# Kernel optimization log

Hardware: AMD Instinct MI355X
Metric: run time of the kernel (lower is better)

Reference implementation:

```python
import jax, jax.numpy as jnp
import numpy as np

N_NODES = 100000


def gcn_conv(h, W, b, src, dst, n):
    # h: [N, Fin] -> [N, Fout], GCNConv with symmetric normalization + self-loops
    h = h @ W  # transform first (PyG order): [N, Fout]
    loop = jnp.arange(n, dtype=src.dtype)
    src_sl = jnp.concatenate([src, loop])  # [E+N]
    dst_sl = jnp.concatenate([dst, loop])
    deg = jax.ops.segment_sum(jnp.ones_like(dst_sl, dtype=h.dtype), dst_sl, num_segments=n)  # [N]
    dinv = jax.lax.rsqrt(deg)  # deg >= 1 thanks to self-loops
    norm = dinv[src_sl] * dinv[dst_sl]  # [E+N]
    msgs = h[src_sl] * norm[:, None]  # gather + scale: [E+N, Fout]
    out = jax.ops.segment_sum(msgs, dst_sl, num_segments=n)  # scatter-add
    return out + b


def setup_inputs() -> dict:
    key = jax.random.key(0)
    kx, ke, k1, k2 = jax.random.split(key, 4)
    in_dim, hid_dim, out_dim = 512, 128, 40
    x = jax.random.normal(kx, (N_NODES, in_dim), dtype=jnp.float32)
    edge_index = jax.random.randint(ke, (2, 1600000), 0, N_NODES, dtype=jnp.int64)
    s1 = 1.0 / np.sqrt(in_dim)
    s2 = 1.0 / np.sqrt(hid_dim)
    W1 = jax.random.uniform(k1, (in_dim, hid_dim), jnp.float32, -s1, s1)
    b1 = jnp.zeros((hid_dim,), jnp.float32)
    W2 = jax.random.uniform(k2, (hid_dim, out_dim), jnp.float32, -s2, s2)
    b2 = jnp.zeros((out_dim,), jnp.float32)
    return {"x": x, "edge_index": edge_index, "W1": W1, "b1": b1, "W2": W2, "b2": b2}


def reference(x, edge_index, W1, b1, W2, b2):
    src, dst = edge_index[0], edge_index[1]
    n = x.shape[0]
    h = jax.nn.relu(gcn_conv(x, W1, b1, src, dst, n))
    h = gcn_conv(h, W2, b2, src, dst, n)
    return jax.nn.log_softmax(h, axis=1)
```

## Files before the change

kernel.cpp:

```cpp
#include <hip/hip_runtime.h>
#include <math.h>

#define FIN 512
#define FH 128
#define FOUT 40
#define FP 64
#define NB 512
#define PSLOTS 30
#define CAPG 4096
#define PBLK 512

typedef unsigned char u8;
typedef __attribute__((ext_vector_type(8))) short bf16x8;
typedef __attribute__((ext_vector_type(4))) float f32x4;
typedef __attribute__((ext_vector_type(2))) float f32x2;

__device__ inline ushort f2bf(float f){
  union { float f; uint32_t u; } v; v.f = f;
  uint32_t u = v.u;
  uint32_t r = (u + 0x7FFF + ((u >> 16) & 1)) >> 16;
  return (ushort)r;
}
__device__ inline uint32_t cvtpk(float a, float b){
  uint32_t r;
  asm("v_cvt_pk_bf16_f32 %0, %1, %2" : "=v"(r) : "v"(a), "v"(b));
  return r;
}
__device__ inline f32x2 pkadd(f32x2 a, f32x2 b){
  f32x2 r;
  asm("v_pk_add_f32 %0, %1, %2" : "=v"(r) : "v"(a), "v"(b));
  return r;
}
__device__ inline f32x2 f8lo(uint32_t v){ return __builtin_amdgcn_cvt_pk_f32_fp8(v, false); }
__device__ inline f32x2 f8hi(uint32_t v){ return __builtin_amdgcn_cvt_pk_f32_fp8(v, true); }
__device__ inline u8 f2f8(float v){
  return (u8)(__builtin_amdgcn_cvt_pk_fp8_f32(v, v, 0, false) & 0xFF);
}

__global__ __launch_bounds__(256) void k_part(const int* __restrict__ src,
                                              const int* __restrict__ dst, int e,
                                              int* __restrict__ gcur,
                                              uint32_t* __restrict__ gbuf, int n, int npb,
                                              const float* __restrict__ W1,
                                              const float* __restrict__ W2,
                                              ushort* __restrict__ W1t, ushort* __restrict__ W2t){
  __shared__ uint32_t pbuf[NB*PSLOTS];
  __shared__ int lcnt[NB];
  int b = blockIdx.x, t = threadIdx.x;
  int gidx = b*256 + t;
  if(gidx < FIN*FH){
    int k = gidx / FH, c = gidx % FH;
    W1t[(size_t)c*FIN + k] = f2bf(W1[gidx]);
  }
  if(gidx < 48*FH){
    int c = gidx / FH, k = gidx % FH;
    W2t[gidx] = (c < FOUT) ? f2bf(W2[(size_t)k*FOUT + c]) : (ushort)0;
  }
  for(int i=t;i<NB;i+=256) lcnt[i]=0;
  __syncthreads();
  int chunk = (e + PBLK - 1) / PBLK;
  int base = b * chunk;
  int endE = base + chunk; if(endE > e) endE = e;
  if(base >= e) return;
  int rounds = (endE - base + 255) / 256;
  for(int rr=0; rr<rounds; ++rr){
    int i = base + rr*256 + t;
    if(i < endE){
      int s = src[i];
      int d = dst[i];
      int bk = d / npb;
      uint32_t pk_ = ((uint32_t)s << 8) | (uint32_t)(d - bk*npb);
      int slot = atomicAdd(&lcnt[bk], 1);
      if(slot < PSLOTS){
        pbuf[bk*PSLOTS + slot] = pk_;
      } else {
        int g = atomicAdd(&gcur[bk], 1);
        gbuf[(size_t)bk*CAPG + g] = pk_;
      }
    }
    __syncthreads();
    bool last = (rr == rounds-1);
    for(int tb=t; tb<NB; tb+=256){
      int c = lcnt[tb];
      int k = c < PSLOTS ? c : PSLOTS;
      if(k > 0 && (k >= 16 || last)){
        int g = atomicAdd(&gcur[tb], k);
        uint32_t* dstp = &gbuf[(size_t)tb*CAPG + g];
        const uint32_t* srcp = &pbuf[tb*PSLOTS];
        for(int q=0; q<k; q++) dstp[q] = srcp[q];
        lcnt[tb] = 0;
      }
    }
    __syncthreads();
  }
}

__global__ __launch_bounds__(256) void k_hist(const uint32_t* __restrict__ gbuf,
                                              const int* __restrict__ gcur,
                                              int* __restrict__ rp, float* __restrict__ dinv,
                                              int* __restrict__ aux, int n, int npb){
  __shared__ int hist[256];
  __shared__ int sh[256];
  int b = blockIdx.x, t = threadIdx.x;
  int base = b * npb;
  if(base >= n){ if(t==0) aux[b] = 0; return; }
  hist[t] = 0;
  __syncthreads();
  int m = gcur[b];
  const uint32_t* bp = gbuf + (size_t)b*CAPG;
  for(int i=t; i<m; i+=256) atomicAdd(&hist[bp[i] & 255u], 1);
  __syncthreads();
  int v = hist[t];
  sh[t] = v;
  __syncthreads();
  for(int off=1; off<256; off<<=1){
    int x = (t>=off)? sh[t-off]:0; __syncthreads();
    sh[t]+=x; __syncthreads();
  }
  int nn = n - base; if(nn > npb) nn = npb;
  if(t < nn){
    rp[base+t+1] = sh[t];
    dinv[base+t] = rsqrtf((float)(v+1));
  }
  if(t==255) aux[b] = sh[255];
}

__global__ __launch_bounds__(512) void k_scan_c(int* __restrict__ rp, const int* __restrict__ aux,
                                                int n, int npb){
  __shared__ int sh[512];
  int t = threadIdx.x;
  sh[t] = aux[t];
  __syncthreads();
  for(int off=1; off<512; off<<=1){
    int x = (t>=off)? sh[t-off]:0; __syncthreads();
    sh[t]+=x; __syncthreads();
  }
  int i = blockIdx.x*512 + t;
  if(i<n){
    int b = i / npb;
    int add = (b>0)? sh[b-1] : 0;
    rp[i+1] += add;
  }
  if(i==0) rp[0] = 0;
}

__global__ __launch_bounds__(512, 2) void k_gemm1(const float* __restrict__ X,
                                                  const ushort* __restrict__ W1t,
                                                  const float* __restrict__ dinv,
                                                  u8* __restrict__ XWs, int n){
  __shared__ char smem[65536];
  int t = threadIdx.x;
  int gi = blockIdx.x;
  int lane = t & 63;
  int wid = t >> 6;
  int l15 = lane & 15;
  int lk8 = (lane >> 4) * 8;
  int rowbase = gi * 256 + wid * 32;

  int r0 = rowbase + l15;      if (r0 >= n) r0 = n-1;
  int r1 = rowbase + 16 + l15; if (r1 >= n) r1 = n-1;
  const float* a0p = X + (size_t)r0*FIN;
  const float* a1p = X + (size_t)r1*FIN;

  f32x4 acc[2][8];
  #pragma unroll
  for(int i=0;i<2;i++)
    #pragma unroll
    for(int j=0;j<8;j++) acc[i][j] = (f32x4){0.f,0.f,0.f,0.f};

  char* WsB = smem;

  #pragma unroll
  for(int half=0; half<2; half++){
    if(half) __syncthreads();
    #pragma unroll
    for(int it=0; it<8; it++){
      int c = it*512 + t;
      int col = c >> 5, kslot = c & 31;
      uint4 v = *(const uint4*)(W1t + (size_t)col*FIN + half*256 + kslot*8);
      int dstb = col*512 + ((kslot*16) ^ ((col & 7) << 4));
      *(uint4*)(WsB + dstb) = v;
    }
    __syncthreads();

    for(int kc=0; kc<8; kc++){
      int kl = kc*32 + lk8;
      int kg = half*256 + kl;
      float4 a0a = *(const float4*)(a0p + kg);
      float4 a0b = *(const float4*)(a0p + kg + 4);
      float4 a1a = *(const float4*)(a1p + kg);
      float4 a1b = *(const float4*)(a1p + kg + 4);
      uint4 fa0u, fa1u;
      fa0u.x = cvtpk(a0a.x, a0a.y); fa0u.y = cvtpk(a0a.z, a0a.w);
      fa0u.z = cvtpk(a0b.x, a0b.y); fa0u.w = cvtpk(a0b.z, a0b.w);
      fa1u.x = cvtpk(a1a.x, a1a.y); fa1u.y = cvtpk(a1a.z, a1a.w);
      fa1u.z = cvtpk(a1b.x, a1b.y); fa1u.w = cvtpk(a1b.z, a1b.w);
      bf16x8 fa0 = *(bf16x8*)&fa0u;
      bf16x8 fa1 = *(bf16x8*)&fa1u;

      #pragma unroll
      for(int fj=0; fj<8; fj++){
        int col = fj*16 + l15;
        int srcb = col*512 + ((kl*2) ^ ((col & 7) << 4));
        bf16x8 fb = *(const bf16x8*)(WsB + srcb);
        acc[0][fj] = __builtin_amdgcn_mfma_f32_16x16x32_bf16(fa0, fb, acc[0][fj], 0, 0, 0);
        acc[1][fj] = __builtin_amdgcn_mfma_f32_16x16x32_bf16(fa1, fb, acc[1][fj], 0, 0, 0);
      }
    }
  }

  int rbase = (lane >> 4) * 4;
  #pragma unroll
  for(int fi=0; fi<2; fi++){
    #pragma unroll
    for(int r=0; r<4; r++){
      int row = rowbase + fi*16 + rbase + r;
      if(row < n){
        float dd = dinv[row];
        #pragma unroll
        for(int fj=0; fj<8; fj++){
          XWs[(size_t)row*FH + fj*16 + l15] = f2f8(acc[fi][fj][r] * dd);
        }
      }
    }
  }
}

__global__ __launch_bounds__(512) void k_fill2(const uint32_t* __restrict__ gbuf,
                                               const int* __restrict__ gcur,
                                               const int* __restrict__ rp,
                                               int* __restrict__ srcs, int n, int npb){
  __shared__ int lcur[256];
  int fb = blockIdx.x;
  int t = threadIdx.x;
  int base = fb * npb;
  if(base >= n) return;
  int nn = n - base; if(nn > npb) nn = npb;
  for(int i = t; i < nn; i += 512) lcur[i] = rp[base + i];
  __syncthreads();
  int m = gcur[fb];
  const uint32_t* bp = gbuf + (size_t)fb*CAPG;
  for(int i = t; i < m; i += 512){
    uint32_t v = bp[i];
    int ld = (int)(v & 255u);
    int p = atomicAdd(&lcur[ld], 1);
    srcs[p] = (int)(v >> 8);
  }
}

__global__ __launch_bounds__(256) void k_agg1(const u8* __restrict__ XWs, const int* __restrict__ rp,
                                              const int* __restrict__ srcs, const float* __restrict__ dinv,
                                              const float* __restrict__ b1, ushort* __restrict__ H1b, int n){
  int d = blockIdx.x*4 + (threadIdx.x >> 6);
  if(d >= n) return;
  int lane = threadIdx.x & 63;
  int g = lane >> 3, li = lane & 7;
  f32x2 acc[8];
  #pragma unroll
  for(int k=0;k<8;k++) acc[k] = (f32x2){0.f,0.f};
  int beg = rp[d];
  int end = rp[d+1];
  int j = beg + g;
  bool h0 = j < end, h1 = j + 8 < end;
  int s0 = 0, s1 = 0;
  if(h0) s0 = srcs[j];
  if(h1) s1 = srcs[j+8];
  while(h1){
    int nj = j + 16;
    bool nh0 = nj < end, nh1 = nj + 8 < end;
    int ns0 = 0, ns1 = 0;
    if(nh0) ns0 = srcs[nj];
    if(nh1) ns1 = srcs[nj+8];
    uint4 a0 = *(const uint4*)(XWs + (size_t)s0*FH + li*16);
    uint4 c0 = *(const uint4*)(XWs + (size_t)s1*FH + li*16);
    acc[0] = pkadd(acc[0], pkadd(f8lo(a0.x), f8lo(c0.x)));
    acc[1] = pkadd(acc[1], pkadd(f8hi(a0.x), f8hi(c0.x)));
    acc[2] = pkadd(acc[2], pkadd(f8lo(a0.y), f8lo(c0.y)));
    acc[3] = pkadd(acc[3], pkadd(f8hi(a0.y), f8hi(c0.y)));
    acc[4] = pkadd(acc[4], pkadd(f8lo(a0.z), f8lo(c0.z)));
    acc[5] = pkadd(acc[5], pkadd(f8hi(a0.z), f8hi(c0.z)));
    acc[6] = pkadd(acc[6], pkadd(f8lo(a0.w), f8lo(c0.w)));
    acc[7] = pkadd(acc[7], pkadd(f8hi(a0.w), f8hi(c0.w)));
    j = nj; s0 = ns0; s1 = ns1; h0 = nh0; h1 = nh1;
  }
  if(h0){
    uint4 a0 = *(const uint4*)(XWs + (size_t)s0*FH + li*16);
    acc[0] = pkadd(acc[0], f8lo(a0.x));
    acc[1] = pkadd(acc[1], f8hi(a0.x));
    acc[2] = pkadd(acc[2], f8lo(a0.y));
    acc[3] = pkadd(acc[3], f8hi(a0.y));
    acc[4] = pkadd(acc[4], f8lo(a0.z));
    acc[5] = pkadd(acc[5], f8hi(a0.z));
    acc[6] = pkadd(acc[6], f8lo(a0.w));
    acc[7] = pkadd(acc[7], f8hi(a0.w));
  }
  #pragma unroll
  for(int k=0;k<8;k++){
    #pragma unroll
    for(int c=0;c<2;c++){
      acc[k][c] += __shfl_xor(acc[k][c], 8);
      acc[k][c] += __shfl_xor(acc[k][c], 16);
      acc[k][c] += __shfl_xor(acc[k][c], 32);
    }
  }
  if(g == 0){
    uint4 sv4 = *(const uint4*)(XWs + (size_t)d*FH + li*16);
    f32x2 slf[8];
    slf[0]=f8lo(sv4.x); slf[1]=f8hi(sv4.x); slf[2]=f8lo(sv4.y); slf[3]=f8hi(sv4.y);
    slf[4]=f8lo(sv4.z); slf[5]=f8hi(sv4.z); slf[6]=f8lo(sv4.w); slf[7]=f8hi(sv4.w);
    float dd = dinv[d];
    uint32_t w[8];
    #pragma unroll
    for(int k=0;k<8;k++){
      float b0 = b1[li*16 + k*2];
      float b1v = b1[li*16 + k*2 + 1];
      float o0 = fmaxf((acc[k][0]+slf[k][0])*dd + b0, 0.f);
      float o1 = fmaxf((acc[k][1]+slf[k][1])*dd + b1v, 0.f);
      w[k] = cvtpk(o0, o1);
    }
    uint4 w0 = {w[0],w[1],w[2],w[3]};
    uint4 w1 = {w[4],w[5],w[6],w[7]};
    uint4* wp = (uint4*)(H1b + (size_t)d*FH + li*16);
    wp[0] = w0;
    wp[1] = w1;
  }
}

__global__ __launch_bounds__(256) void k_gemm2_mfma(const ushort* __restrict__ H1b,
                                                    const ushort* __restrict__ W2t,
                                                    const float* __restrict__ dinv,
                                                    u8* __restrict__ H2s, int n){
  int t = threadIdx.x;
  int lane = t & 63;
  int wid = t >> 6;
  int l15 = lane & 15;
  int lk8 = (lane >> 4) * 8;
  int rowbase = blockIdx.x * 128 + wid * 32;

  int r0 = rowbase + l15;      if (r0 >= n) r0 = n-1;
  int r1 = rowbase + 16 + l15; if (r1 >= n) r1 = n-1;
  const ushort* a0p = H1b + (size_t)r0*FH + lk8;
  const ushort* a1p = H1b + (size_t)r1*FH + lk8;

  f32x4 acc[2][3];
  #pragma unroll
  for(int i=0;i<2;i++)
    #pragma unroll
    for(int j=0;j<3;j++) acc[i][j] = (f32x4){0.f,0.f,0.f,0.f};

  #pragma unroll
  for(int kc=0; kc<4; kc++){
    int k0 = kc*32;
    bf16x8 fa0 = *(const bf16x8*)(a0p + k0);
    bf16x8 fa1 = *(const bf16x8*)(a1p + k0);
    #pragma unroll
    for(int fj=0; fj<3; fj++){
      bf16x8 fb = *(const bf16x8*)(W2t + (size_t)(fj*16 + l15)*FH + k0 + lk8);
      acc[0][fj] = __builtin_amdgcn_mfma_f32_16x16x32_bf16(fa0, fb, acc[0][fj], 0, 0, 0);
      acc[1][fj] = __builtin_amdgcn_mfma_f32_16x16x32_bf16(fa1, fb, acc[1][fj], 0, 0, 0);
    }
  }

  int rbase = (lane >> 4) * 4;
  #pragma unroll
  for(int fi=0; fi<2; fi++){
    #pragma unroll
    for(int r=0; r<4; r++){
      int row = rowbase + fi*16 + rbase + r;
      if(row < n){
        float dd = dinv[row];
        #pragma unroll
        for(int fj=0; fj<3; fj++){
          int col = fj*16 + l15;
          H2s[(size_t)row*FP + col] = (col < FOUT) ? f2f8(acc[fi][fj][r] * dd) : (u8)0;
        }
        H2s[(size_t)row*FP + 48 + l15] = (u8)0;
      }
    }
  }
}

__global__ __launch_bounds__(256) void k_agg2_sm(const u8* __restrict__ H2s, const int* __restrict__ rp,
                                                 const int* __restrict__ srcs, const float* __restrict__ dinv,
                                                 const float* __restrict__ b2, float* __restrict__ out, int n){
  int d = blockIdx.x*4 + (threadIdx.x >> 6);
  if(d >= n) return;
  int lane = threadIdx.x & 63;
  int g = lane >> 3, li = lane & 7;
  f32x2 acc[4];
  #pragma unroll
  for(int k=0;k<4;k++) acc[k] = (f32x2){0.f,0.f};
  int beg = rp[d];
  int end = rp[d+1];
  int j = beg + g;
  bool h0 = j < end, h1 = j + 8 < end;
  int s0 = 0, s1 = 0;
  if(h0) s0 = srcs[j];
  if(h1) s1 = srcs[j+8];
  while(h1){
    int nj = j + 16;
    bool nh0 = nj < end, nh1 = nj + 8 < end;
    int ns0 = 0, ns1 = 0;
    if(nh0) ns0 = srcs[nj];
    if(nh1) ns1 = srcs[nj+8];
    uint2 v = *(const uint2*)(H2s + (size_t)s0*FP + li*8);
    uint2 u = *(const uint2*)(H2s + (size_t)s1*FP + li*8);
    acc[0] = pkadd(acc[0], pkadd(f8lo(v.x), f8lo(u.x)));
    acc[1] = pkadd(acc[1], pkadd(f8hi(v.x), f8hi(u.x)));
    acc[2] = pkadd(acc[2], pkadd(f8lo(v.y), f8lo(u.y)));
    acc[3] = pkadd(acc[3], pkadd(f8hi(v.y), f8hi(u.y)));
    j = nj; s0 = ns0; s1 = ns1; h0 = nh0; h1 = nh1;
  }
  if(h0){
    uint2 v = *(const uint2*)(H2s + (size_t)s0*FP + li*8);
    acc[0] = pkadd(acc[0], f8lo(v.x));
    acc[1] = pkadd(acc[1], f8hi(v.x));
    acc[2] = pkadd(acc[2], f8lo(v.y));
    acc[3] = pkadd(acc[3], f8hi(v.y));
  }
  #pragma unroll
  for(int k=0;k<4;k++){
    #pragma unroll
    for(int c=0;c<2;c++){
      acc[k][c] += __shfl_xor(acc[k][c], 8);
      acc[k][c] += __shfl_xor(acc[k][c], 16);
      acc[k][c] += __shfl_xor(acc[k][c], 32);
    }
  }
  uint2 sv = *(const uint2*)(H2s + (size_t)d*FP + li*8);
  f32x2 s2[4] = { f8lo(sv.x), f8hi(sv.x), f8lo(sv.y), f8hi(sv.y) };
  float dd = dinv[d];
  float val[8];
  #pragma unroll
  for(int k=0;k<4;k++){
    #pragma unroll
    for(int c=0;c<2;c++){
      int col = li*8 + k*2 + c;
      float bv = (col < FOUT) ? b2[col] : 0.f;
      val[k*2+c] = (col < FOUT) ? ((acc[k][c]+s2[k][c])*dd + bv) : -3.402823466e38f;
    }
  }
  float m = val[0];
  #pragma unroll
  for(int k=1;k<8;k++) m = fmaxf(m, val[k]);
  #pragma unroll
  for(int off=1; off<8; off<<=1) m = fmaxf(m, __shfl_xor(m, off));
  float ssum = 0.f;
  #pragma unroll
  for(int k=0;k<8;k++){
    int col = li*8 + k;
    ssum += (col < FOUT) ? expf(val[k] - m) : 0.f;
  }
  #pragma unroll
  for(int off=1; off<8; off<<=1) ssum += __shfl_xor(ssum, off);
  float lse = m + logf(ssum);
  if(g == 0 && li < 5){
    float4 o0 = {val[0]-lse, val[1]-lse, val[2]-lse, val[3]-lse};
    float4 o1 = {val[4]-lse, val[5]-lse, val[6]-lse, val[7]-lse};
    float* op = out + (size_t)d*FOUT + li*8;
    *(float4*)op = o0;
    *(float4*)(op+4) = o1;
  }
}


extern "C" void kernel_launch(void* const* d_in, const int* in_sizes, int n_in,
                              void* d_out, int out_size, void* d_ws, size_t ws_size,
                              hipStream_t stream){
  const float* X  = (const float*)d_in[0];
  const int*   ei = (const int*)d_in[1];
  const float* W1 = (const float*)d_in[2];
  const float* b1 = (const float*)d_in[3];
  const float* W2 = (const float*)d_in[4];
  const float* b2 = (const float*)d_in[5];
  float* out = (float*)d_out;

  int n = in_sizes[0] / FIN;
  int e = in_sizes[1] / 2;
  const int* src = ei;
  const int* dst = ei + e;

  int npb = (n + NB - 1) / NB;

  u8* XWs     = (u8*)d_ws;
  ushort* H1b = (ushort*)(XWs + (size_t)n*FH);
  u8* H2s     = (u8*)(H1b + (size_t)n*FH);
  ushort* W1t = (ushort*)(H2s + (size_t)n*FP);
  ushort* W2t = W1t + (size_t)FH*FIN;
  float* dinv = (float*)(W2t + 48*FH);
  int* gcur   = (int*)(dinv + n);
  int* rp     = gcur + NB;
  int* srcs   = rp + (n+1) + 3;
  int* aux    = srcs + e;
  uint32_t* gbuf = (uint32_t*)H1b;

  int G = (n + 255) / 256;

  hipMemsetAsync(gcur, 0, (size_t)NB*sizeof(int), stream);
  hipLaunchKernelGGL(k_part, dim3(PBLK), dim3(256), 0, stream,
                     src, dst, e, gcur, gbuf, n, npb, W1, W2, W1t, W2t);
  hipLaunchKernelGGL(k_hist, dim3(NB), dim3(256), 0, stream, gbuf, gcur, rp, dinv, aux, n, npb);
  hipLaunchKernelGGL(k_scan_c, dim3((n+511)/512), dim3(512), 0, stream, rp, aux, n, npb);

  hipLaunchKernelGGL(k_gemm1, dim3(G), dim3(512), 0, stream, X, W1t, dinv, XWs, n);
  hipLaunchKernelGGL(k_fill2, dim3(NB), dim3(512), 0, stream, gbuf, gcur, rp, srcs, n, npb);

  hipLaunchKernelGGL(k_agg1, dim3((n+3)/4), dim3(256), 0, stream, XWs, rp, srcs, dinv, b1, H1b, n);
  hipLaunchKernelGGL(k_gemm2_mfma, dim3((n+127)/128), dim3(256), 0, stream, H1b, W2t, dinv, H2s, n);
  hipLaunchKernelGGL(k_agg2_sm, dim3((n+3)/4), dim3(256), 0, stream, H2s, rp, srcs, dinv, b2, out, n);
}
```

Baseline: 247.9 us.

## Simplify edge partition to direct global atomics and fuse histogram with CSR fill

The partition kernel drops its shared-memory staging buffers. Each edge now goes straight into its dst bucket in the global buffer through a global atomic, using one thread per edge. The block-offset scan now runs on the bucket counts in a single small kernel, and the per-bucket histogram is fused with the CSR source fill, removing the separate scan and fill launches. This cuts launches and a pass over the bucket buffer, but adds heavy global atomic contention on 512 counters across 1.6M edges.

```diff
diff --git a/kernel.cpp b/kernel.cpp
--- a/kernel.cpp
+++ b/kernel.cpp
@@ -6,9 +6,7 @@
 #define FOUT 40
 #define FP 64
 #define NB 512
-#define PSLOTS 30
 #define CAPG 4096
-#define PBLK 512
 
 typedef unsigned char u8;
 typedef __attribute__((ext_vector_type(8))) short bf16x8;
@@ -44,66 +42,50 @@
                                               const float* __restrict__ W1,
                                               const float* __restrict__ W2,
                                               ushort* __restrict__ W1t, ushort* __restrict__ W2t){
-  __shared__ uint32_t pbuf[NB*PSLOTS];
-  __shared__ int lcnt[NB];
-  int b = blockIdx.x, t = threadIdx.x;
-  int gidx = b*256 + t;
-  if(gidx < FIN*FH){
-    int k = gidx / FH, c = gidx % FH;
-    W1t[(size_t)c*FIN + k] = f2bf(W1[gidx]);
-  }
-  if(gidx < 48*FH){
-    int c = gidx / FH, k = gidx % FH;
-    W2t[gidx] = (c < FOUT) ? f2bf(W2[(size_t)k*FOUT + c]) : (ushort)0;
-  }
-  for(int i=t;i<NB;i+=256) lcnt[i]=0;
+  int i = blockIdx.x*256 + threadIdx.x;
+  if(i < FIN*FH){
+    int k = i / FH, c = i % FH;
+    W1t[(size_t)c*FIN + k] = f2bf(W1[i]);
+  }
+  if(i < 48*FH){
+    int c = i / FH, k = i % FH;
+    W2t[i] = (c < FOUT) ? f2bf(W2[(size_t)k*FOUT + c]) : (ushort)0;
+  }
+  if(i < e){
+    int s = src[i];
+    int d = dst[i];
+    int bk = d / npb;
+    uint32_t pk_ = ((uint32_t)s << 8) | (uint32_t)(d - bk*npb);
+    int p = atomicAdd(&gcur[bk], 1);
+    gbuf[(size_t)bk*CAPG + p] = pk_;
+  }
+}
+
+__global__ __launch_bounds__(512) void k_scan_g(const int* __restrict__ gcur,
+                                                int* __restrict__ bstart){
+  __shared__ int sh[512];
+  int t = threadIdx.x;
+  sh[t] = gcur[t];
   __syncthreads();
-  int chunk = (e + PBLK - 1) / PBLK;
-  int base = b * chunk;
-  int endE = base + chunk; if(endE > e) endE = e;
-  if(base >= e) return;
-  int rounds = (endE - base + 255) / 256;
-  for(int rr=0; rr<rounds; ++rr){
-    int i = base + rr*256 + t;
-    if(i < endE){
-      int s = src[i];
-      int d = dst[i];
-      int bk = d / npb;
-      uint32_t pk_ = ((uint32_t)s << 8) | (uint32_t)(d - bk*npb);
-      int slot = atomicAdd(&lcnt[bk], 1);
-      if(slot < PSLOTS){
-        pbuf[bk*PSLOTS + slot] = pk_;
-      } else {
-        int g = atomicAdd(&gcur[bk], 1);
-        gbuf[(size_t)bk*CAPG + g] = pk_;
-      }
-    }
-    __syncthreads();
-    bool last = (rr == rounds-1);
-    for(int tb=t; tb<NB; tb+=256){
-      int c = lcnt[tb];
-      int k = c < PSLOTS ? c : PSLOTS;
-      if(k > 0 && (k >= 16 || last)){
-        int g = atomicAdd(&gcur[tb], k);
-        uint32_t* dstp = &gbuf[(size_t)tb*CAPG + g];
-        const uint32_t* srcp = &pbuf[tb*PSLOTS];
-        for(int q=0; q<k; q++) dstp[q] = srcp[q];
-        lcnt[tb] = 0;
-      }
-    }
-    __syncthreads();
-  }
-}
-
-__global__ __launch_bounds__(256) void k_hist(const uint32_t* __restrict__ gbuf,
-                                              const int* __restrict__ gcur,
-                                              int* __restrict__ rp, float* __restrict__ dinv,
-                                              int* __restrict__ aux, int n, int npb){
+  for(int off=1; off<512; off<<=1){
+    int x = (t>=off)? sh[t-off]:0; __syncthreads();
+    sh[t]+=x; __syncthreads();
+  }
+  bstart[t] = (t>0)? sh[t-1] : 0;
+}
+
+__global__ __launch_bounds__(256) void k_histfill(const uint32_t* __restrict__ gbuf,
+                                                  const int* __restrict__ gcur,
+                                                  const int* __restrict__ bstart,
+                                                  int* __restrict__ rp, float* __restrict__ dinv,
+                                                  int* __restrict__ srcs, int n, int npb){
   __shared__ int hist[256];
   __shared__ int sh[256];
+  __shared__ int lcur[256];
   int b = blockIdx.x, t = threadIdx.x;
   int base = b * npb;
-  if(base >= n){ if(t==0) aux[b] = 0; return; }
+  if(base >= n) return;
+  int nn = n - base; if(nn > npb) nn = npb;
   hist[t] = 0;
   __syncthreads();
   int m = gcur[b];
@@ -117,31 +99,20 @@
     int x = (t>=off)? sh[t-off]:0; __syncthreads();
     sh[t]+=x; __syncthreads();
   }
-  int nn = n - base; if(nn > npb) nn = npb;
+  int bs = bstart[b];
   if(t < nn){
-    rp[base+t+1] = sh[t];
+    rp[base+t+1] = bs + sh[t];
     dinv[base+t] = rsqrtf((float)(v+1));
-  }
-  if(t==255) aux[b] = sh[255];
-}
-
-__global__ __launch_bounds__(512) void k_scan_c(int* __restrict__ rp, const int* __restrict__ aux,
-                                                int n, int npb){
-  __shared__ int sh[512];
-  int t = threadIdx.x;
-  sh[t] = aux[t];
+    lcur[t] = bs + sh[t] - v;
+  }
+  if(b==0 && t==0) rp[0] = 0;
   __syncthreads();
-  for(int off=1; off<512; off<<=1){
-    int x = (t>=off)? sh[t-off]:0; __syncthreads();
-    sh[t]+=x; __syncthreads();
-  }
-  int i = blockIdx.x*512 + t;
-  if(i<n){
-    int b = i / npb;
-    int add = (b>0)? sh[b-1] : 0;
-    rp[i+1] += add;
-  }
-  if(i==0) rp[0] = 0;
+  for(int i=t; i<m; i+=256){
+    uint32_t w = bp[i];
+    int ld = (int)(w & 255u);
+    int p = atomicAdd(&lcur[ld], 1);
+    srcs[p] = (int)(w >> 8);
+  }
 }
 
 __global__ __launch_bounds__(512, 2) void k_gemm1(const float* __restrict__ X,
@@ -223,28 +194,6 @@
         }
       }
     }
-  }
-}
-
-__global__ __launch_bounds__(512) void k_fill2(const uint32_t* __restrict__ gbuf,
-                                               const int* __restrict__ gcur,
-                                               const int* __restrict__ rp,
-                                               int* __restrict__ srcs, int n, int npb){
-  __shared__ int lcur[256];
-  int fb = blockIdx.x;
-  int t = threadIdx.x;
-  int base = fb * npb;
-  if(base >= n) return;
-  int nn = n - base; if(nn > npb) nn = npb;
-  for(int i = t; i < nn; i += 512) lcur[i] = rp[base + i];
-  __syncthreads();
-  int m = gcur[fb];
-  const uint32_t* bp = gbuf + (size_t)fb*CAPG;
-  for(int i = t; i < m; i += 512){
-    uint32_t v = bp[i];
-    int ld = (int)(v & 255u);
-    int p = atomicAdd(&lcur[ld], 1);
-    srcs[p] = (int)(v >> 8);
   }
 }
 
@@ -489,21 +438,21 @@
   ushort* W2t = W1t + (size_t)FH*FIN;
   float* dinv = (float*)(W2t + 48*FH);
   int* gcur   = (int*)(dinv + n);
-  int* rp     = gcur + NB;
+  int* bstart = gcur + NB;
+  int* rp     = bstart + NB;
   int* srcs   = rp + (n+1) + 3;
-  int* aux    = srcs + e;
   uint32_t* gbuf = (uint32_t*)H1b;
 
   int G = (n + 255) / 256;
 
   hipMemsetAsync(gcur, 0, (size_t)NB*sizeof(int), stream);
-  hipLaunchKernelGGL(k_part, dim3(PBLK), dim3(256), 0, stream,
+  hipLaunchKernelGGL(k_part, dim3((e+255)/256), dim3(256), 0, stream,
                      src, dst, e, gcur, gbuf, n, npb, W1, W2, W1t, W2t);
-  hipLaunchKernelGGL(k_hist, dim3(NB), dim3(256), 0, stream, gbuf, gcur, rp, dinv, aux, n, npb);
-  hipLaunchKernelGGL(k_scan_c, dim3((n+511)/512), dim3(512), 0, stream, rp, aux, n, npb);
+  hipLaunchKernelGGL(k_scan_g, dim3(1), dim3(512), 0, stream, gcur, bstart);
+  hipLaunchKernelGGL(k_histfill, dim3(NB), dim3(256), 0, stream,
+                     gbuf, gcur, bstart, rp, dinv, srcs, n, npb);
 
   hipLaunchKernelGGL(k_gemm1, dim3(G), dim3(512), 0, stream, X, W1t, dinv, XWs, n);
-  hipLaunchKernelGGL(k_fill2, dim3(NB), dim3(512), 0, stream, gbuf, gcur, rp, srcs, n, npb);
 
   hipLaunchKernelGGL(k_agg1, dim3((n+3)/4), dim3(256), 0, stream, XWs, rp, srcs, dinv, b1, H1b, n);
   hipLaunchKernelGGL(k_gemm2_mfma, dim3((n+127)/128), dim3(256), 0, stream, H1b, W2t, dinv, H2s, n);
```

Result: slower. 698.5 us (+181.8%).

## Fuse histogram, scan fixup and CSR fill into one kernel

Applied to the files above, without the earlier changes.

A single-block kernel now scans the per-bucket counts first, giving each bucket its global start offset. The histogram kernel then writes final row pointers directly and, in the same launch, scatters source indices into the CSR array from shared-memory cursors. This removes the separate row-pointer fixup pass and the standalone fill kernel, along with one launch and a re-read of the bucket buffer. The fill loop now runs with 256 threads instead of 512, and a tiny single-block launch sits on the critical path.

```diff
diff --git a/kernel.cpp b/kernel.cpp
--- a/kernel.cpp
+++ b/kernel.cpp
@@ -95,15 +95,31 @@
   }
 }
 
-__global__ __launch_bounds__(256) void k_hist(const uint32_t* __restrict__ gbuf,
-                                              const int* __restrict__ gcur,
-                                              int* __restrict__ rp, float* __restrict__ dinv,
-                                              int* __restrict__ aux, int n, int npb){
+__global__ __launch_bounds__(512) void k_scan_g(const int* __restrict__ gcur,
+                                                int* __restrict__ bstart){
+  __shared__ int sh[512];
+  int t = threadIdx.x;
+  sh[t] = gcur[t];
+  __syncthreads();
+  for(int off=1; off<512; off<<=1){
+    int x = (t>=off)? sh[t-off]:0; __syncthreads();
+    sh[t]+=x; __syncthreads();
+  }
+  bstart[t] = (t>0)? sh[t-1] : 0;
+}
+
+__global__ __launch_bounds__(256) void k_histfill(const uint32_t* __restrict__ gbuf,
+                                                  const int* __restrict__ gcur,
+                                                  const int* __restrict__ bstart,
+                                                  int* __restrict__ rp, float* __restrict__ dinv,
+                                                  int* __restrict__ srcs, int n, int npb){
   __shared__ int hist[256];
   __shared__ int sh[256];
+  __shared__ int lcur[256];
   int b = blockIdx.x, t = threadIdx.x;
   int base = b * npb;
-  if(base >= n){ if(t==0) aux[b] = 0; return; }
+  if(base >= n) return;
+  int nn = n - base; if(nn > npb) nn = npb;
   hist[t] = 0;
   __syncthreads();
   int m = gcur[b];
@@ -117,31 +133,20 @@
     int x = (t>=off)? sh[t-off]:0; __syncthreads();
     sh[t]+=x; __syncthreads();
   }
-  int nn = n - base; if(nn > npb) nn = npb;
+  int bs = bstart[b];
   if(t < nn){
-    rp[base+t+1] = sh[t];
+    rp[base+t+1] = bs + sh[t];
     dinv[base+t] = rsqrtf((float)(v+1));
-  }
-  if(t==255) aux[b] = sh[255];
-}
-
-__global__ __launch_bounds__(512) void k_scan_c(int* __restrict__ rp, const int* __restrict__ aux,
-                                                int n, int npb){
-  __shared__ int sh[512];
-  int t = threadIdx.x;
-  sh[t] = aux[t];
-  __syncthreads();
-  for(int off=1; off<512; off<<=1){
-    int x = (t>=off)? sh[t-off]:0; __syncthreads();
-    sh[t]+=x; __syncthreads();
-  }
-  int i = blockIdx.x*512 + t;
-  if(i<n){
-    int b = i / npb;
-    int add = (b>0)? sh[b-1] : 0;
-    rp[i+1] += add;
-  }
-  if(i==0) rp[0] = 0;
+    lcur[t] = bs + sh[t] - v;
+  }
+  if(b==0 && t==0) rp[0] = 0;
+  __syncthreads();
+  for(int i=t; i<m; i+=256){
+    uint32_t w = bp[i];
+    int ld = (int)(w & 255u);
+    int p = atomicAdd(&lcur[ld], 1);
+    srcs[p] = (int)(w >> 8);
+  }
 }
 
 __global__ __launch_bounds__(512, 2) void k_gemm1(const float* __restrict__ X,
@@ -223,28 +228,6 @@
         }
       }
     }
-  }
-}
-
-__global__ __launch_bounds__(512) void k_fill2(const uint32_t* __restrict__ gbuf,
-                                               const int* __restrict__ gcur,
-                                               const int* __restrict__ rp,
-                                               int* __restrict__ srcs, int n, int npb){
-  __shared__ int lcur[256];
-  int fb = blockIdx.x;
-  int t = threadIdx.x;
-  int base = fb * npb;
-  if(base >= n) return;
-  int nn = n - base; if(nn > npb) nn = npb;
-  for(int i = t; i < nn; i += 512) lcur[i] = rp[base + i];
-  __syncthreads();
-  int m = gcur[fb];
-  const uint32_t* bp = gbuf + (size_t)fb*CAPG;
-  for(int i = t; i < m; i += 512){
-    uint32_t v = bp[i];
-    int ld = (int)(v & 255u);
-    int p = atomicAdd(&lcur[ld], 1);
-    srcs[p] = (int)(v >> 8);
   }
 }
 
@@ -489,9 +472,9 @@
   ushort* W2t = W1t + (size_t)FH*FIN;
   float* dinv = (float*)(W2t + 48*FH);
   int* gcur   = (int*)(dinv + n);
-  int* rp     = gcur + NB;
+  int* bstart = gcur + NB;
+  int* rp     = bstart + NB;
   int* srcs   = rp + (n+1) + 3;
-  int* aux    = srcs + e;
   uint32_t* gbuf = (uint32_t*)H1b;
 
   int G = (n + 255) / 256;
@@ -499,11 +482,11 @@
   hipMemsetAsync(gcur, 0, (size_t)NB*sizeof(int), stream);
   hipLaunchKernelGGL(k_part, dim3(PBLK), dim3(256), 0, stream,
                      src, dst, e, gcur, gbuf, n, npb, W1, W2, W1t, W2t);
-  hipLaunchKernelGGL(k_hist, dim3(NB), dim3(256), 0, stream, gbuf, gcur, rp, dinv, aux, n, npb);
-  hipLaunchKernelGGL(k_scan_c, dim3((n+511)/512), dim3(512), 0, stream, rp, aux, n, npb);
+  hipLaunchKernelGGL(k_scan_g, dim3(1), dim3(512), 0, stream, gcur, bstart);
+  hipLaunchKernelGGL(k_histfill, dim3(NB), dim3(256), 0, stream,
+                     gbuf, gcur, bstart, rp, dinv, srcs, n, npb);
 
   hipLaunchKernelGGL(k_gemm1, dim3(G), dim3(512), 0, stream, X, W1t, dinv, XWs, n);
-  hipLaunchKernelGGL(k_fill2, dim3(NB), dim3(512), 0, stream, gbuf, gcur, rp, srcs, n, npb);
 
   hipLaunchKernelGGL(k_agg1, dim3((n+3)/4), dim3(256), 0, stream, XWs, rp, srcs, dinv, b1, H1b, n);
   hipLaunchKernelGGL(k_gemm2_mfma, dim3((n+127)/128), dim3(256), 0, stream, H1b, W2t, dinv, H2s, n);
```

Result: no change. 244.8 us (-1.3%).
